# Kernel optimization log

Hardware: AMD Instinct MI355X
Metric: run time of the kernel (lower is better)

## Reference

```python
import jax, jax.numpy as jnp
import numpy as np

N_HEAD = 8
N_EMBD = 768
T_MAX = 1024


def setup_inputs() -> dict:
    key = jax.random.key(0)
    ks = jax.random.split(key, 5)
    B, T, C = 8, 1024, N_EMBD
    x = jax.random.normal(ks[0], (B, T, C), dtype=jnp.float32)
    c_attn_weight = jax.random.normal(ks[1], (3 * C, C), dtype=jnp.float32) * (1.0 / np.sqrt(C))
    c_attn_bias = jax.random.normal(ks[2], (3 * C,), dtype=jnp.float32) * 0.02
    c_proj_weight = jax.random.normal(ks[3], (C, C), dtype=jnp.float32) * (1.0 / np.sqrt(C))
    c_proj_bias = jax.random.normal(ks[4], (C,), dtype=jnp.float32) * 0.02
    bias = jnp.tril(jnp.ones((T_MAX, T_MAX), dtype=jnp.int32))[None, None]  # (1,1,Tmax,Tmax)
    return {
        "x": x,
        "c_attn_weight": c_attn_weight,
        "c_attn_bias": c_attn_bias,
        "c_proj_weight": c_proj_weight,
        "c_proj_bias": c_proj_bias,
        "bias": bias,
    }


def reference(x, c_attn_weight, c_attn_bias, c_proj_weight, c_proj_bias, bias):
    B, T, C = x.shape
    H = N_HEAD
    D = C // H  # head dim
    qkv = jnp.einsum("btc,fc->btf", x, c_attn_weight) + c_attn_bias  # (B,T,3C)
    q, k, v = jnp.split(qkv, 3, axis=-1)
    q = q.reshape(B, T, H, D).transpose(0, 2, 1, 3)  # (B,H,T,D)
    k = k.reshape(B, T, H, D).transpose(0, 2, 1, 3)
    v = v.reshape(B, T, H, D).transpose(0, 2, 1, 3)
    att = jnp.einsum("bhqd,bhkd->bhqk", q, k) * (1.0 / np.sqrt(D))  # (B,H,T,T)
    mask = bias[:, :, :T, :T] == 0
    att = jnp.where(mask, jnp.float32(-jnp.inf), att)
    att = jax.nn.softmax(att, axis=-1)
    y = jnp.einsum("bhqk,bhkd->bhqd", att, v)  # (B,H,T,D)
    y = y.transpose(0, 2, 1, 3).reshape(B, T, C)
    y = jnp.einsum("btc,fc->btf", y, c_proj_weight) + c_proj_bias
    return y
```

## Files before the change

kernel.cpp:

```cpp
#include <hip/hip_runtime.h>
#include <hip/hip_bf16.h>
#include <stdint.h>


typedef unsigned short ushort_t;
typedef __attribute__((ext_vector_type(8))) short short8;
typedef __attribute__((ext_vector_type(4))) float floatx4;
typedef __attribute__((ext_vector_type(4))) unsigned short ushort4v;

#define MFMA16(a, b, c) __builtin_amdgcn_mfma_f32_16x16x32_bf16(a, b, c, 0, 0, 0)
#define NEG_BIG (-1e30f)

__device__ __forceinline__ unsigned short f2bf(float f) {
  union { float f; unsigned int u; } v; v.f = f;
  unsigned int r = (v.u + 0x7FFFu + ((v.u >> 16) & 1u)) >> 16;
  return (unsigned short)r;
}

__device__ __forceinline__ unsigned int packbf2(float a, float b) {
  union { __hip_bfloat162 h; unsigned int u; } cv;
  cv.h = __float22bfloat162_rn(make_float2(a, b));
  return cv.u;
}

__global__ __launch_bounds__(256) void cvt3(
    const float* __restrict__ x, const float* __restrict__ wa,
    const float* __restrict__ wp, ushort_t* __restrict__ xb,
    ushort_t* __restrict__ wab, ushort_t* __restrict__ wpb)
{
  const int n1 = (8192 * 768) / 4, n2 = (2304 * 768) / 4;
  int i = blockIdx.x * 256 + threadIdx.x;
  const float* in; ushort_t* out;
  if (i < n1)            { in = x;  out = xb; }
  else if (i < n1 + n2)  { in = wa; out = wab; i -= n1; }
  else                   { in = wp; out = wpb; i -= (n1 + n2); }
  float4 v = *(const float4*)(in + (size_t)i * 4);
  ushort4v o;
  o.x = f2bf(v.x); o.y = f2bf(v.y); o.z = f2bf(v.z); o.w = f2bf(v.w);
  *(ushort4v*)(out + (size_t)i * 4) = o;
}

__global__ __launch_bounds__(256) void gemm_qkv(
    const ushort_t* __restrict__ A,
    const ushort_t* __restrict__ W,
    const float* __restrict__ bias,
    ushort_t* __restrict__ QK,
    ushort_t* __restrict__ VT)
{
  const int K = 768;
  __shared__ ushort_t As[128 * 32];
  __shared__ ushort_t Bs[128 * 32];

  const int tid  = threadIdx.x;
  const int lane = tid & 63;
  const int l15  = lane & 15;
  const int quad = lane >> 4;
  const int wid  = tid >> 6;
  const int m0 = blockIdx.x * 128;
  const int n0 = blockIdx.y * 128;
  const int wm = (wid >> 1) * 64;
  const int wn = (wid & 1) * 64;
  const int srow = tid >> 2;
  const int scol = (tid & 3) * 8;

  floatx4 acc[4][4] = {};

  const ushort_t* gA = A + (size_t)(m0 + srow) * K + scol;
  const ushort_t* gB = W + (size_t)(n0 + srow) * K + scol;
  ushort_t* lA = &As[wid * 512];
  ushort_t* lB = &Bs[wid * 512];

  for (int k0 = 0; k0 < K; k0 += 32) {
    __builtin_amdgcn_global_load_lds(
        (const __attribute__((address_space(1))) void*)gA,
        (__attribute__((address_space(3))) void*)lA, 16, 0, 0);
    __builtin_amdgcn_global_load_lds(
        (const __attribute__((address_space(1))) void*)(gA + (size_t)64 * K),
        (__attribute__((address_space(3))) void*)(lA + 64 * 32), 16, 0, 0);
    __builtin_amdgcn_global_load_lds(
        (const __attribute__((address_space(1))) void*)gB,
        (__attribute__((address_space(3))) void*)lB, 16, 0, 0);
    __builtin_amdgcn_global_load_lds(
        (const __attribute__((address_space(1))) void*)(gB + (size_t)64 * K),
        (__attribute__((address_space(3))) void*)(lB + 64 * 32), 16, 0, 0);
    gA += 32; gB += 32;
    __syncthreads();

    short8 af[4], bf[4];
#pragma unroll
    for (int t = 0; t < 4; ++t)
      af[t] = *(const short8*)&As[(wm + t * 16 + l15) * 32 + quad * 8];
#pragma unroll
    for (int t = 0; t < 4; ++t)
      bf[t] = *(const short8*)&Bs[(wn + t * 16 + l15) * 32 + quad * 8];
#pragma unroll
    for (int tm = 0; tm < 4; ++tm)
#pragma unroll
      for (int tn = 0; tn < 4; ++tn)
        acc[tm][tn] = MFMA16(af[tm], bf[tn], acc[tm][tn]);
    __syncthreads();
  }

  const float QSCALE = 0.10206207261596577f * 1.4426950408889634f;

#pragma unroll
  for (int tn = 0; tn < 4; ++tn) {
    const int gc = n0 + wn + tn * 16 + l15;
    const float bv = bias[gc];
    const bool isv = (gc >= 1536);
    const bool isq = (gc < 768);
    const int hh = (gc - 1536) / 96, dd = (gc - 1536) % 96;
#pragma unroll
    for (int tm = 0; tm < 4; ++tm) {
      const int gr = m0 + wm + tm * 16 + quad * 4;
#pragma unroll
      for (int r = 0; r < 4; ++r) {
        float val = acc[tm][tn][r] + bv;
        const int row = gr + r;
        if (!isv) {
          if (isq) val *= QSCALE;
          QK[(size_t)row * 1536 + gc] = f2bf(val);
        } else {
          const int bb = row >> 10, tt = row & 1023;
          const int tt2 = (tt & ~0x1C) | (((tt >> 4) & 1) << 2) |
                          (((tt >> 2) & 3) << 3);
          VT[(((size_t)(bb * 8 + hh)) * 96 + dd) * 1024 + tt2] = f2bf(val);
        }
      }
    }
  }
}

__global__ __launch_bounds__(256) void gemm_proj(
    const ushort_t* __restrict__ A,
    const ushort_t* __restrict__ W,
    const float* __restrict__ bias,
    float* __restrict__ C,
    int M, int N, int K)
{
  __shared__ ushort_t As[128 * 32];
  __shared__ ushort_t Bs[128 * 32];

  const int tid  = threadIdx.x;
  const int lane = tid & 63;
  const int l15  = lane & 15;
  const int quad = lane >> 4;
  const int wid  = tid >> 6;
  const int m0 = blockIdx.x * 128;
  const int n0 = blockIdx.y * 128;
  const int wm = (wid >> 1) * 64;
  const int wn = (wid & 1) * 64;
  const int srow = tid >> 2;
  const int scol = (tid & 3) * 8;

  floatx4 acc[4][4] = {};

  const ushort_t* gA = A + (size_t)(m0 + srow) * K + scol;
  const ushort_t* gB = W + (size_t)(n0 + srow) * K + scol;
  ushort_t* lA = &As[wid * 512];
  ushort_t* lB = &Bs[wid * 512];

  for (int k0 = 0; k0 < K; k0 += 32) {
    __builtin_amdgcn_global_load_lds(
        (const __attribute__((address_space(1))) void*)gA,
        (__attribute__((address_space(3))) void*)lA, 16, 0, 0);
    __builtin_amdgcn_global_load_lds(
        (const __attribute__((address_space(1))) void*)(gA + (size_t)64 * K),
        (__attribute__((address_space(3))) void*)(lA + 64 * 32), 16, 0, 0);
    __builtin_amdgcn_global_load_lds(
        (const __attribute__((address_space(1))) void*)gB,
        (__attribute__((address_space(3))) void*)lB, 16, 0, 0);
    __builtin_amdgcn_global_load_lds(
        (const __attribute__((address_space(1))) void*)(gB + (size_t)64 * K),
        (__attribute__((address_space(3))) void*)(lB + 64 * 32), 16, 0, 0);
    gA += 32; gB += 32;
    __syncthreads();

    short8 af[4], bf[4];
#pragma unroll
    for (int t = 0; t < 4; ++t)
      af[t] = *(const short8*)&As[(wm + t * 16 + l15) * 32 + quad * 8];
#pragma unroll
    for (int t = 0; t < 4; ++t)
      bf[t] = *(const short8*)&Bs[(wn + t * 16 + l15) * 32 + quad * 8];
#pragma unroll
    for (int tm = 0; tm < 4; ++tm)
#pragma unroll
      for (int tn = 0; tn < 4; ++tn)
        acc[tm][tn] = MFMA16(af[tm], bf[tn], acc[tm][tn]);
    __syncthreads();
  }

#pragma unroll
  for (int tn = 0; tn < 4; ++tn) {
    const int gc = n0 + wn + tn * 16 + l15;
    const float bv = bias[gc];
#pragma unroll
    for (int tm = 0; tm < 4; ++tm) {
      const int gr = m0 + wm + tm * 16 + quad * 4;
#pragma unroll
      for (int r = 0; r < 4; ++r)
        C[(size_t)(gr + r) * N + gc] = acc[tm][tn][r] + bv;
    }
  }
}

__global__ __launch_bounds__(256) void attn_fused(
    const ushort_t* __restrict__ QK,
    const ushort_t* __restrict__ VT,
    ushort_t* __restrict__ y)
{
  __shared__ ushort_t Ks[64 * 96];
  __shared__ ushort_t Vt[96 * 72];

  const int tid  = threadIdx.x;
  const int lane = tid & 63;
  const int l15  = lane & 15;
  const int quad = lane >> 4;
  const int wid  = tid >> 6;
  const int bh = blockIdx.y;
  const int b = bh >> 3;
  const int h = bh & 7;
  const int qoff = h * 96;

  const int cA = blockIdx.x;
  const int cB = 31 - cA;
  const int myChunk = (wid < 2) ? cA : cB;
  const int q0w = myChunk * 32 + (wid & 1) * 16;
  const int kend = cB * 32 + 32;
  const int rq = q0w + l15;

  const size_t rowbase = (size_t)b * 1024;
  const ushort_t* vtb = VT + (size_t)bh * 96 * 1024;

  short8 qf[3];
#pragma unroll
  for (int c = 0; c < 3; ++c)
    qf[c] = *(const short8*)(QK + (rowbase + q0w + l15) * 1536 + qoff +
                             c * 32 + quad * 8);

  float m_i = NEG_BIG;
  float l_i = 0.f;
  floatx4 O[6] = {};

  for (int k0 = 0; k0 < kend; k0 += 64) {
#pragma unroll
    for (int i = 0; i < 3; ++i) {
      const int e = wid * 1536 + i * 512 + lane * 8;
      const int kr = e / 96, kc = e % 96;
      __builtin_amdgcn_global_load_lds(
          (const __attribute__((address_space(1))) void*)
              (QK + (rowbase + k0 + kr) * 1536 + 768 + qoff + kc),
          (__attribute__((address_space(3))) void*)(&Ks[wid * 1536 + i * 512]),
          16, 0, 0);
    }
#pragma unroll
    for (int g = 0; g < 3; ++g) {
      const int d = g * 32 + (tid >> 3);
      const int kc = (tid & 7) * 8;
      short8 v = *(const short8*)(vtb + (size_t)d * 1024 + k0 + kc);
      *(short8*)&Vt[d * 72 + kc] = v;
    }
    __syncthreads();

    if (k0 < q0w + 16) {
      floatx4 s[4] = {};
#pragma unroll
      for (int t = 0; t < 4; ++t) {
#pragma unroll
        for (int c = 0; c < 3; ++c) {
          short8 kf = *(const short8*)&Ks[(t * 16 + l15) * 96 + c * 32 + quad * 8];
          s[t] = MFMA16(kf, qf[c], s[t]);
        }
      }
      float p[4][4];
      if (k0 + 64 <= q0w) {
#pragma unroll
        for (int t = 0; t < 4; ++t)
#pragma unroll
          for (int j = 0; j < 4; ++j) p[t][j] = s[t][j];
      } else {
        const int kq = k0 + quad * 4;
#pragma unroll
        for (int t = 0; t < 4; ++t)
#pragma unroll
          for (int j = 0; j < 4; ++j)
            p[t][j] = (kq + t * 16 + j <= rq) ? s[t][j] : NEG_BIG;
      }
      float m0v = fmaxf(fmaxf(p[0][0], p[0][1]), fmaxf(p[0][2], p[0][3]));
      float m1v = fmaxf(fmaxf(p[1][0], p[1][1]), fmaxf(p[1][2], p[1][3]));
      float m2v = fmaxf(fmaxf(p[2][0], p[2][1]), fmaxf(p[2][2], p[2][3]));
      float m3v = fmaxf(fmaxf(p[3][0], p[3][1]), fmaxf(p[3][2], p[3][3]));
      float mt = fmaxf(fmaxf(m0v, m1v), fmaxf(m2v, m3v));
      mt = fmaxf(mt, __shfl_xor(mt, 16));
      mt = fmaxf(mt, __shfl_xor(mt, 32));
      if (!__all(mt - m_i <= 8.0f)) {
        const float mn = fmaxf(m_i, mt);
        const float al = __builtin_amdgcn_exp2f(m_i - mn);
        m_i = mn;
        l_i *= al;
#pragma unroll
        for (int j = 0; j < 4; ++j) {
          const float alr = __shfl(al, quad * 4 + j);
#pragma unroll
          for (int f = 0; f < 6; ++f) O[f][j] *= alr;
        }
      }
      float rs = 0.f;
#pragma unroll
      for (int t = 0; t < 4; ++t)
#pragma unroll
        for (int j = 0; j < 4; ++j) {
          p[t][j] = __builtin_amdgcn_exp2f(p[t][j] - m_i);
          rs += p[t][j];
        }
      rs += __shfl_xor(rs, 16);
      rs += __shfl_xor(rs, 32);
      l_i += rs;
      union { short8 s8; unsigned int u[4]; } pf0, pf1;
      pf0.u[0] = packbf2(p[0][0], p[0][1]);
      pf0.u[1] = packbf2(p[0][2], p[0][3]);
      pf0.u[2] = packbf2(p[1][0], p[1][1]);
      pf0.u[3] = packbf2(p[1][2], p[1][3]);
      pf1.u[0] = packbf2(p[2][0], p[2][1]);
      pf1.u[1] = packbf2(p[2][2], p[2][3]);
      pf1.u[2] = packbf2(p[3][0], p[3][1]);
      pf1.u[3] = packbf2(p[3][2], p[3][3]);
#pragma unroll
      for (int f = 0; f < 6; ++f) {
        short8 vf0 = *(const short8*)&Vt[(f * 16 + l15) * 72 + quad * 8];
        O[f] = MFMA16(pf0.s8, vf0, O[f]);
        short8 vf1 = *(const short8*)&Vt[(f * 16 + l15) * 72 + 32 + quad * 8];
        O[f] = MFMA16(pf1.s8, vf1, O[f]);
      }
    }
    __syncthreads();
  }

  float inv[4];
#pragma unroll
  for (int j = 0; j < 4; ++j) {
    const float lj = __shfl(l_i, quad * 4 + j);
    inv[j] = 1.0f / fmaxf(lj, 1e-20f);
  }
#pragma unroll
  for (int j = 0; j < 4; ++j) {
    const size_t row = rowbase + q0w + quad * 4 + j;
#pragma unroll
    for (int f = 0; f < 6; ++f)
      y[row * 768 + qoff + f * 16 + l15] = f2bf(O[f][j] * inv[j]);
  }
}

extern "C" void kernel_launch(void* const* d_in, const int* in_sizes, int n_in,
                              void* d_out, int out_size, void* d_ws, size_t ws_size,
                              hipStream_t stream)
{
  const float* x_f  = (const float*)d_in[0];
  const float* wa_f = (const float*)d_in[1];
  const float* ba_f = (const float*)d_in[2];
  const float* wp_f = (const float*)d_in[3];
  const float* bp_f = (const float*)d_in[4];
  float* out = (float*)d_out;

  ushort_t* xb  = (ushort_t*)d_ws;
  ushort_t* wab = xb  + (size_t)8192 * 768;
  ushort_t* wpb = wab + (size_t)2304 * 768;
  ushort_t* QK  = wpb + (size_t)768 * 768;
  ushort_t* VT  = QK  + (size_t)8192 * 1536;
  ushort_t* yw  = VT  + (size_t)8192 * 768;

  cvt3<<<8448, 256, 0, stream>>>(x_f, wa_f, wp_f, xb, wab, wpb);

  gemm_qkv<<<dim3(64, 18), 256, 0, stream>>>(xb, wab, ba_f, QK, VT);
  attn_fused<<<dim3(16, 64), 256, 0, stream>>>(QK, VT, yw);
  gemm_proj<<<dim3(64, 6), 256, 0, stream>>>(yw, wpb, bp_f, out,
                                             8192, 768, 768);
}
```

Baseline: 230.5 us.

## Double-buffer LDS tiles in QKV, proj GEMMs and attention to overlap loads

Adds two-stage LDS buffers to both GEMM kernels and the fused attention kernel. The next K/V or A/B tile is issued before the MFMA work on the current tile, leaving one barrier per iteration. V is staged through registers and written to LDS after compute. The aim is to hide global-load latency behind MFMA work, at the cost of double the LDS use (which may lower occupancy) and extra registers for the V prefetch.

```diff
diff --git a/kernel.cpp b/kernel.cpp
--- a/kernel.cpp
+++ b/kernel.cpp
@@ -22,6 +22,11 @@
   cv.h = __float22bfloat162_rn(make_float2(a, b));
   return cv.u;
 }
+
+#define GLOAD16(src, dst)                                              \
+  __builtin_amdgcn_global_load_lds(                                    \
+      (const __attribute__((address_space(1))) void*)(src),            \
+      (__attribute__((address_space(3))) void*)(dst), 16, 0, 0)
 
 __global__ __launch_bounds__(256) void cvt3(
     const float* __restrict__ x, const float* __restrict__ wa,
@@ -48,8 +53,8 @@
     ushort_t* __restrict__ VT)
 {
   const int K = 768;
-  __shared__ ushort_t As[128 * 32];
-  __shared__ ushort_t Bs[128 * 32];
+  __shared__ ushort_t As[2][128 * 32];
+  __shared__ ushort_t Bs[2][128 * 32];
 
   const int tid  = threadIdx.x;
   const int lane = tid & 63;
@@ -67,38 +72,44 @@
 
   const ushort_t* gA = A + (size_t)(m0 + srow) * K + scol;
   const ushort_t* gB = W + (size_t)(n0 + srow) * K + scol;
-  ushort_t* lA = &As[wid * 512];
-  ushort_t* lB = &Bs[wid * 512];
-
+
+  {
+    ushort_t* lA = &As[0][wid * 512];
+    ushort_t* lB = &Bs[0][wid * 512];
+    GLOAD16(gA, lA);
+    GLOAD16(gA + (size_t)64 * K, lA + 64 * 32);
+    GLOAD16(gB, lB);
+    GLOAD16(gB + (size_t)64 * K, lB + 64 * 32);
+  }
+  __syncthreads();
+
+  int cur = 0;
   for (int k0 = 0; k0 < K; k0 += 32) {
-    __builtin_amdgcn_global_load_lds(
-        (const __attribute__((address_space(1))) void*)gA,
-        (__attribute__((address_space(3))) void*)lA, 16, 0, 0);
-    __builtin_amdgcn_global_load_lds(
-        (const __attribute__((address_space(1))) void*)(gA + (size_t)64 * K),
-        (__attribute__((address_space(3))) void*)(lA + 64 * 32), 16, 0, 0);
-    __builtin_amdgcn_global_load_lds(
-        (const __attribute__((address_space(1))) void*)gB,
-        (__attribute__((address_space(3))) void*)lB, 16, 0, 0);
-    __builtin_amdgcn_global_load_lds(
-        (const __attribute__((address_space(1))) void*)(gB + (size_t)64 * K),
-        (__attribute__((address_space(3))) void*)(lB + 64 * 32), 16, 0, 0);
-    gA += 32; gB += 32;
-    __syncthreads();
+    if (k0 + 32 < K) {
+      ushort_t* lA = &As[cur ^ 1][wid * 512];
+      ushort_t* lB = &Bs[cur ^ 1][wid * 512];
+      const ushort_t* pA = gA + k0 + 32;
+      const ushort_t* pB = gB + k0 + 32;
+      GLOAD16(pA, lA);
+      GLOAD16(pA + (size_t)64 * K, lA + 64 * 32);
+      GLOAD16(pB, lB);
+      GLOAD16(pB + (size_t)64 * K, lB + 64 * 32);
+    }
 
     short8 af[4], bf[4];
 #pragma unroll
     for (int t = 0; t < 4; ++t)
-      af[t] = *(const short8*)&As[(wm + t * 16 + l15) * 32 + quad * 8];
+      af[t] = *(const short8*)&As[cur][(wm + t * 16 + l15) * 32 + quad * 8];
 #pragma unroll
     for (int t = 0; t < 4; ++t)
-      bf[t] = *(const short8*)&Bs[(wn + t * 16 + l15) * 32 + quad * 8];
+      bf[t] = *(const short8*)&Bs[cur][(wn + t * 16 + l15) * 32 + quad * 8];
 #pragma unroll
     for (int tm = 0; tm < 4; ++tm)
 #pragma unroll
       for (int tn = 0; tn < 4; ++tn)
         acc[tm][tn] = MFMA16(af[tm], bf[tn], acc[tm][tn]);
     __syncthreads();
+    cur ^= 1;
   }
 
   const float QSCALE = 0.10206207261596577f * 1.4426950408889634f;
@@ -138,8 +149,8 @@
     float* __restrict__ C,
     int M, int N, int K)
 {
-  __shared__ ushort_t As[128 * 32];
-  __shared__ ushort_t Bs[128 * 32];
+  __shared__ ushort_t As[2][128 * 32];
+  __shared__ ushort_t Bs[2][128 * 32];
 
   const int tid  = threadIdx.x;
   const int lane = tid & 63;
@@ -157,38 +168,44 @@
 
   const ushort_t* gA = A + (size_t)(m0 + srow) * K + scol;
   const ushort_t* gB = W + (size_t)(n0 + srow) * K + scol;
-  ushort_t* lA = &As[wid * 512];
-  ushort_t* lB = &Bs[wid * 512];
-
+
+  {
+    ushort_t* lA = &As[0][wid * 512];
+    ushort_t* lB = &Bs[0][wid * 512];
+    GLOAD16(gA, lA);
+    GLOAD16(gA + (size_t)64 * K, lA + 64 * 32);
+    GLOAD16(gB, lB);
+    GLOAD16(gB + (size_t)64 * K, lB + 64 * 32);
+  }
+  __syncthreads();
+
+  int cur = 0;
   for (int k0 = 0; k0 < K; k0 += 32) {
-    __builtin_amdgcn_global_load_lds(
-        (const __attribute__((address_space(1))) void*)gA,
-        (__attribute__((address_space(3))) void*)lA, 16, 0, 0);
-    __builtin_amdgcn_global_load_lds(
-        (const __attribute__((address_space(1))) void*)(gA + (size_t)64 * K),
-        (__attribute__((address_space(3))) void*)(lA + 64 * 32), 16, 0, 0);
-    __builtin_amdgcn_global_load_lds(
-        (const __attribute__((address_space(1))) void*)gB,
-        (__attribute__((address_space(3))) void*)lB, 16, 0, 0);
-    __builtin_amdgcn_global_load_lds(
-        (const __attribute__((address_space(1))) void*)(gB + (size_t)64 * K),
-        (__attribute__((address_space(3))) void*)(lB + 64 * 32), 16, 0, 0);
-    gA += 32; gB += 32;
-    __syncthreads();
+    if (k0 + 32 < K) {
+      ushort_t* lA = &As[cur ^ 1][wid * 512];
+      ushort_t* lB = &Bs[cur ^ 1][wid * 512];
+      const ushort_t* pA = gA + k0 + 32;
+      const ushort_t* pB = gB + k0 + 32;
+      GLOAD16(pA, lA);
+      GLOAD16(pA + (size_t)64 * K, lA + 64 * 32);
+      GLOAD16(pB, lB);
+      GLOAD16(pB + (size_t)64 * K, lB + 64 * 32);
+    }
 
     short8 af[4], bf[4];
 #pragma unroll
     for (int t = 0; t < 4; ++t)
-      af[t] = *(const short8*)&As[(wm + t * 16 + l15) * 32 + quad * 8];
+      af[t] = *(const short8*)&As[cur][(wm + t * 16 + l15) * 32 + quad * 8];
 #pragma unroll
     for (int t = 0; t < 4; ++t)
-      bf[t] = *(const short8*)&Bs[(wn + t * 16 + l15) * 32 + quad * 8];
+      bf[t] = *(const short8*)&Bs[cur][(wn + t * 16 + l15) * 32 + quad * 8];
 #pragma unroll
     for (int tm = 0; tm < 4; ++tm)
 #pragma unroll
       for (int tn = 0; tn < 4; ++tn)
         acc[tm][tn] = MFMA16(af[tm], bf[tn], acc[tm][tn]);
     __syncthreads();
+    cur ^= 1;
   }
 
 #pragma unroll
@@ -210,8 +227,8 @@
     const ushort_t* __restrict__ VT,
     ushort_t* __restrict__ y)
 {
-  __shared__ ushort_t Ks[64 * 96];
-  __shared__ ushort_t Vt[96 * 72];
+  __shared__ ushort_t Ks[2][64 * 96];
+  __shared__ ushort_t Vt[2][96 * 72];
 
   const int tid  = threadIdx.x;
   const int lane = tid & 63;
@@ -233,6 +250,10 @@
   const size_t rowbase = (size_t)b * 1024;
   const ushort_t* vtb = VT + (size_t)bh * 96 * 1024;
 
+  const int ke0 = wid * 1536 + lane * 8;
+  const int vd  = (tid >> 3);
+  const int vkc = (tid & 7) * 8;
+
   short8 qf[3];
 #pragma unroll
   for (int c = 0; c < 3; ++c)
@@ -243,25 +264,41 @@
   float l_i = 0.f;
   floatx4 O[6] = {};
 
+  {
+#pragma unroll
+    for (int i = 0; i < 3; ++i) {
+      const int e = ke0 + i * 512;
+      const int kr = e / 96, kc = e % 96;
+      GLOAD16(QK + (rowbase + kr) * 1536 + 768 + qoff + kc,
+              &Ks[0][wid * 1536 + i * 512]);
+    }
+#pragma unroll
+    for (int g = 0; g < 3; ++g) {
+      const int d = g * 32 + vd;
+      short8 v = *(const short8*)(vtb + (size_t)d * 1024 + vkc);
+      *(short8*)&Vt[0][d * 72 + vkc] = v;
+    }
+  }
+  __syncthreads();
+
+  int cur = 0;
   for (int k0 = 0; k0 < kend; k0 += 64) {
-#pragma unroll
-    for (int i = 0; i < 3; ++i) {
-      const int e = wid * 1536 + i * 512 + lane * 8;
-      const int kr = e / 96, kc = e % 96;
-      __builtin_amdgcn_global_load_lds(
-          (const __attribute__((address_space(1))) void*)
-              (QK + (rowbase + k0 + kr) * 1536 + 768 + qoff + kc),
-          (__attribute__((address_space(3))) void*)(&Ks[wid * 1536 + i * 512]),
-          16, 0, 0);
-    }
-#pragma unroll
-    for (int g = 0; g < 3; ++g) {
-      const int d = g * 32 + (tid >> 3);
-      const int kc = (tid & 7) * 8;
-      short8 v = *(const short8*)(vtb + (size_t)d * 1024 + k0 + kc);
-      *(short8*)&Vt[d * 72 + kc] = v;
-    }
-    __syncthreads();
+    const int nk = k0 + 64;
+    const bool more = (nk < kend);
+
+    short8 vreg[3];
+    if (more) {
+#pragma unroll
+      for (int i = 0; i < 3; ++i) {
+        const int e = ke0 + i * 512;
+        const int kr = e / 96, kc = e % 96;
+        GLOAD16(QK + (rowbase + nk + kr) * 1536 + 768 + qoff + kc,
+                &Ks[cur ^ 1][wid * 1536 + i * 512]);
+      }
+#pragma unroll
+      for (int g = 0; g < 3; ++g)
+        vreg[g] = *(const short8*)(vtb + (size_t)(g * 32 + vd) * 1024 + nk + vkc);
+    }
 
     if (k0 < q0w + 16) {
       floatx4 s[4] = {};
@@ -269,7 +306,8 @@
       for (int t = 0; t < 4; ++t) {
 #pragma unroll
         for (int c = 0; c < 3; ++c) {
-          short8 kf = *(const short8*)&Ks[(t * 16 + l15) * 96 + c * 32 + quad * 8];
+          short8 kf = *(const short8*)
+              &Ks[cur][(t * 16 + l15) * 96 + c * 32 + quad * 8];
           s[t] = MFMA16(kf, qf[c], s[t]);
         }
       }
@@ -328,13 +366,21 @@
       pf1.u[3] = packbf2(p[3][2], p[3][3]);
 #pragma unroll
       for (int f = 0; f < 6; ++f) {
-        short8 vf0 = *(const short8*)&Vt[(f * 16 + l15) * 72 + quad * 8];
+        short8 vf0 = *(const short8*)&Vt[cur][(f * 16 + l15) * 72 + quad * 8];
         O[f] = MFMA16(pf0.s8, vf0, O[f]);
-        short8 vf1 = *(const short8*)&Vt[(f * 16 + l15) * 72 + 32 + quad * 8];
+        short8 vf1 = *(const short8*)
+            &Vt[cur][(f * 16 + l15) * 72 + 32 + quad * 8];
         O[f] = MFMA16(pf1.s8, vf1, O[f]);
       }
     }
+
+    if (more) {
+#pragma unroll
+      for (int g = 0; g < 3; ++g)
+        *(short8*)&Vt[cur ^ 1][(g * 32 + vd) * 72 + vkc] = vreg[g];
+    }
     __syncthreads();
+    cur ^= 1;
   }
 
   float inv[4];
```

Result: no change. 227.6 us (-1.3%).
